# Kernel optimization log

Measured on AMD Instinct MI355X. Metric: run time of the kernel, lower is better.

The kernel has to match this reference:

```python
import jax, jax.numpy as jnp
import numpy as np

N_ATOMS = 50000
N_RES = 6250
C_IN = 30
E_DIM = 12
E_BOND = 150000
E_RAD = 800000
E_RES_RAD = 400000
E_CORR = 20000


def _layer_norm(h, g, b, eps=1e-5):
    mu = h.mean(-1, keepdims=True)
    var = ((h - mu) ** 2).mean(-1, keepdims=True)
    return (h - mu) / jnp.sqrt(var + eps) * g + b


def _mlp(h, W, b, g, beta):
    # Seq(Linear, ReLU, LayerNorm, Dropout) in eval mode (dropout = identity)
    return _layer_norm(jax.nn.relu(h @ W + b), g, beta)


def _point_conv(x, pos, src, dst, W, b, g, beta, num_nodes):
    # PyG PointNetConv with add_self_loops=True, aggr='add'
    loops = jnp.arange(num_nodes)
    s = jnp.concatenate([src, loops])
    d = jnp.concatenate([dst, loops])
    msg = jnp.concatenate([x[s], pos[s] - pos[d]], axis=-1)  # [E+N, F+3]
    h = _mlp(msg, W, b, g, beta)
    return jax.ops.segment_sum(h, d, num_segments=num_nodes)


def _gcne_conv(x, edge_index, edge_attr, W, bias):
    # GCNEConv: gcn_norm with self loops, message = cat(x_j, e) @ W * norm + bias, scatter-add
    n = x.shape[0]
    loops = jnp.arange(n)
    s = jnp.concatenate([edge_index[0], loops])
    d = jnp.concatenate([edge_index[1], loops])
    w_full = jnp.ones(s.shape[0], x.dtype)
    deg = jax.ops.segment_sum(w_full, d, num_segments=n)
    dinv = jnp.where(deg > 0, deg ** -0.5, 0.0)
    norm = dinv[s] * dinv[d]
    ea = jnp.concatenate([edge_attr, jnp.zeros((n, edge_attr.shape[1]), edge_attr.dtype)], axis=0)
    msg = (jnp.concatenate([x[s], ea], axis=-1) @ W) * norm[:, None] + bias
    return jax.ops.segment_sum(msg, d, num_segments=n)


def setup_inputs():
    key = jax.random.key(0)
    ks = jax.random.split(key, 20)
    inp = {}
    inp['x'] = jax.random.normal(ks[0], (N_ATOMS, C_IN), jnp.float32)
    inp['pos'] = jax.random.uniform(ks[1], (N_ATOMS, 3), jnp.float32)
    inp['edge_attr'] = jax.random.normal(ks[2], (E_BOND, E_DIM), jnp.float32)
    inp['edge_index'] = jax.random.randint(ks[3], (2, E_BOND), 0, N_ATOMS)
    inp['rad_edge_index'] = jax.random.randint(ks[4], (2, E_RAD), 0, N_ATOMS)
    inp['res_rad_edge_index'] = jax.random.randint(ks[5], (2, E_RES_RAD), 0, N_RES)
    inp['residue_index'] = jnp.sort(jax.random.randint(ks[6], (N_ATOMS,), 0, N_RES))
    inp['src_idx'] = jax.random.randint(ks[7], (E_CORR,), 0, N_RES)
    inp['tgt_idx'] = jax.random.randint(ks[8], (E_CORR,), 0, N_RES)
    inp['y_lab'] = jax.random.randint(ks[9], (E_CORR,), 0, 2).astype(jnp.int32)
    def glorot(k, shape):
        s = (2.0 / (shape[0] + shape[1])) ** 0.5
        return jax.random.normal(k, shape, jnp.float32) * s
    # conv1 local MLP [3+C_IN -> 64]
    inp['w_pc1'] = glorot(ks[10], (C_IN + 3, 64)); inp['b_pc1'] = jnp.zeros(64)
    inp['g_pc1'] = jnp.ones(64); inp['be_pc1'] = jnp.zeros(64)
    # gcn1 weight [C_IN+E_DIM -> 64]
    inp['w_gcn'] = glorot(ks[11], (C_IN + E_DIM, 64)); inp['b_gcn'] = jnp.zeros(64)
    # atom_embed MLP [64 -> 64]
    inp['w_ae'] = glorot(ks[12], (64, 64)); inp['b_ae'] = jnp.zeros(64)
    inp['g_ae'] = jnp.ones(64); inp['be_ae'] = jnp.zeros(64)
    # res_embed MLP [64 -> 64]
    inp['w_re'] = glorot(ks[13], (64, 64)); inp['b_re'] = jnp.zeros(64)
    inp['g_re'] = jnp.ones(64); inp['be_re'] = jnp.zeros(64)
    # res_conv1 local MLP [3+64 -> 128]
    inp['w_rc'] = glorot(ks[14], (64 + 3, 128)); inp['b_rc'] = jnp.zeros(128)
    inp['g_rc'] = jnp.ones(128); inp['be_rc'] = jnp.zeros(128)
    # res_conv1 global MLP [128 -> 128]
    inp['w_rg'] = glorot(ks[15], (128, 128)); inp['b_rg'] = jnp.zeros(128)
    inp['g_rg'] = jnp.ones(128); inp['be_rg'] = jnp.zeros(128)
    return inp


def reference(x, pos, edge_attr,
              w_pc1, b_pc1, g_pc1, be_pc1,
              w_gcn, b_gcn,
              w_ae, b_ae, g_ae, be_ae,
              w_re, b_re, g_re, be_re,
              w_rc, b_rc, g_rc, be_rc,
              w_rg, b_rg, g_rg, be_rg,
              edge_index, rad_edge_index, res_rad_edge_index,
              residue_index, src_idx, tgt_idx, y_lab):
    n = x.shape[0]
    # SAModule 1: PointConv over atom radius graph, aggr='add', no global_nn
    x1 = _point_conv(x, pos, rad_edge_index[0], rad_edge_index[1],
                     w_pc1, b_pc1, g_pc1, be_pc1, n)
    # GCNEConv over bond graph
    x2 = _gcne_conv(x, edge_index, edge_attr, w_gcn, b_gcn)
    atom_x = _mlp(x1 + x2, w_ae, b_ae, g_ae, be_ae)
    # atom -> residue pooling (global_add_pool / global_mean_pool)
    res_x = jax.ops.segment_sum(atom_x, residue_index, num_segments=N_RES)
    cnt = jax.ops.segment_sum(jnp.ones(n, x.dtype), residue_index, num_segments=N_RES)
    res_pos = jax.ops.segment_sum(pos, residue_index, num_segments=N_RES) / jnp.maximum(cnt, 1.0)[:, None]
    res_x = _mlp(res_x, w_re, b_re, g_re, be_re)
    # SAModule 2: PointConv over residue radius graph with global MLP
    x3 = _point_conv(res_x, res_pos, res_rad_edge_index[0], res_rad_edge_index[1],
                     w_rc, b_rc, g_rc, be_rc, N_RES)
    x3 = _mlp(x3, w_rg, b_rg, g_rg, be_rg)
    # correspondence pairs + CosineEmbeddingLoss(reduction='none')
    x_s = x3[src_idx]
    x_t = x3[tgt_idx]
    y = (2 * y_lab - 1).astype(x.dtype)  # {0,1} -> {-1,+1}
    eps = 1e-8
    cos = (x_s * x_t).sum(-1) / (jnp.maximum(jnp.linalg.norm(x_s, axis=-1), eps) *
                                 jnp.maximum(jnp.linalg.norm(x_t, axis=-1), eps))
    unweighted = jnp.where(y == 1, 1.0 - cos, jnp.maximum(cos, 0.0))
    pos_l = jnp.where(y != 1, 0.0, y)
    neg_l = 1.0 - pos_l
    pos_w = neg_l.sum() / pos_l.sum()
    loss = jnp.mean((pos_l * pos_w + neg_l) * unweighted)
    return loss
```

## Files before the change

### kernel.cpp

```cpp
#include <hip/hip_runtime.h>
#include <math.h>

#define N_ATOMS 50000
#define N_RES 6250
#define C_IN 30
#define E_DIM 12
#define E_BOND 150000
#define E_RAD 800000
#define E_RES_RAD 400000
#define E_CORR 20000

__device__ __forceinline__ int rfl(int v) { return __builtin_amdgcn_readfirstlane(v); }

template <int K>
__global__ void rowmat64(const float* __restrict__ X, const float* __restrict__ W,
                         float* __restrict__ out, int nrows) {
  const int lane = threadIdx.x & 63;
  const int wid = (blockIdx.x * blockDim.x + threadIdx.x) >> 6;
  const int nw = (gridDim.x * blockDim.x) >> 6;
  float wcol[K];
#pragma unroll
  for (int k = 0; k < K; k++) wcol[k] = W[k * 64 + lane];
  for (int r = wid; r < nrows; r += nw) {
    float acc = 0.0f;
#pragma unroll
    for (int k = 0; k < K; k++) acc += X[(size_t)r * K + k] * wcol[k];
    out[(size_t)r * 64 + lane] = acc;
  }
}

__global__ void hist_kernel(const int* __restrict__ dst, int* __restrict__ cnt, int n) {
  int i = blockIdx.x * blockDim.x + threadIdx.x;
  if (i < n) atomicAdd(&cnt[dst[i]], 1);
}

__global__ void ex_scan(const int* __restrict__ cnt, int* __restrict__ cur, int n) {
  __shared__ int wsums[16];
  __shared__ int carry_s;
  const int tid = threadIdx.x;
  const int lane = tid & 63;
  const int w = tid >> 6;
  if (tid == 0) carry_s = 0;
  __syncthreads();
  for (int base = 0; base < n; base += 1024) {
    int i = base + tid;
    int v = (i < n) ? cnt[i] : 0;
    int s = v;
#pragma unroll
    for (int m = 1; m < 64; m <<= 1) {
      int t = __shfl_up(s, m, 64);
      if (lane >= m) s += t;
    }
    if (lane == 63) wsums[w] = s;
    __syncthreads();
    if (w == 0) {
      int x = (lane < 16) ? wsums[lane] : 0;
#pragma unroll
      for (int m = 1; m < 16; m <<= 1) {
        int t = __shfl_up(x, m, 64);
        if (lane >= m) x += t;
      }
      if (lane < 16) wsums[lane] = x;
    }
    __syncthreads();
    const int woff = (w > 0) ? wsums[w - 1] : 0;
    const int carry = carry_s;
    if (i < n) cur[i] = carry + woff + (s - v);
    __syncthreads();
    if (tid == 1023) carry_s = carry + wsums[15];
    __syncthreads();
  }
}

__global__ void scat_kernel(const int* __restrict__ src, const int* __restrict__ dst,
                            int* __restrict__ cur, int* __restrict__ ss, int n) {
  int e = blockIdx.x * blockDim.x + threadIdx.x;
  if (e < n) {
    int p = atomicAdd(&cur[dst[e]], 1);
    ss[p] = src[e];
  }
}

__global__ void pc1_gather(const float* __restrict__ xw1, const float* __restrict__ pos,
                           const int* __restrict__ ss, const int* __restrict__ cur,
                           const float* __restrict__ W, const float* __restrict__ b,
                           const float* __restrict__ g, const float* __restrict__ be,
                           float* __restrict__ acc) {
  const int lane = threadIdx.x & 63;
  const int d = (blockIdx.x * blockDim.x + threadIdx.x) >> 6;
  if (d >= N_ATOMS) return;
  const float w0 = W[(C_IN + 0) * 64 + lane];
  const float w1 = W[(C_IN + 1) * 64 + lane];
  const float w2 = W[(C_IN + 2) * 64 + lane];
  const float bb = b[lane], gg = g[lane], eb = be[lane];
  const int beg = rfl(d ? cur[d - 1] : 0);
  const int end = rfl(cur[d]);
  const float pd0 = pos[d * 3 + 0], pd1 = pos[d * 3 + 1], pd2 = pos[d * 3 + 2];
  float h = fmaxf(xw1[(size_t)d * 64 + lane] + bb, 0.0f);
  float s1 = h, s2 = h * h;
#pragma unroll
  for (int m = 1; m < 64; m <<= 1) {
    s1 += __shfl_xor(s1, m, 64);
    s2 += __shfl_xor(s2, m, 64);
  }
  float mu = s1 * (1.0f / 64.0f);
  float var = s2 * (1.0f / 64.0f) - mu * mu;
  float accv = (h - mu) * rsqrtf(var + 1e-5f) * gg + eb;
  int j = beg;
  for (; j + 1 < end; j += 2) {
    const int sA = rfl(ss[j]);
    const int sB = rfl(ss[j + 1]);
    const float dA0 = pos[sA * 3 + 0] - pd0, dA1 = pos[sA * 3 + 1] - pd1,
                dA2 = pos[sA * 3 + 2] - pd2;
    const float dB0 = pos[sB * 3 + 0] - pd0, dB1 = pos[sB * 3 + 1] - pd1,
                dB2 = pos[sB * 3 + 2] - pd2;
    float hA = fmaxf(xw1[(size_t)sA * 64 + lane] + bb + dA0 * w0 + dA1 * w1 + dA2 * w2, 0.0f);
    float hB = fmaxf(xw1[(size_t)sB * 64 + lane] + bb + dB0 * w0 + dB1 * w1 + dB2 * w2, 0.0f);
    float s1A = hA, s2A = hA * hA, s1B = hB, s2B = hB * hB;
#pragma unroll
    for (int m = 1; m < 64; m <<= 1) {
      s1A += __shfl_xor(s1A, m, 64);
      s2A += __shfl_xor(s2A, m, 64);
      s1B += __shfl_xor(s1B, m, 64);
      s2B += __shfl_xor(s2B, m, 64);
    }
    const float muA = s1A * (1.0f / 64.0f), muB = s1B * (1.0f / 64.0f);
    const float vaA = s2A * (1.0f / 64.0f) - muA * muA;
    const float vaB = s2B * (1.0f / 64.0f) - muB * muB;
    accv += (hA - muA) * rsqrtf(vaA + 1e-5f) * gg + eb;
    accv += (hB - muB) * rsqrtf(vaB + 1e-5f) * gg + eb;
  }
  if (j < end) {
    const int sA = rfl(ss[j]);
    const float dA0 = pos[sA * 3 + 0] - pd0, dA1 = pos[sA * 3 + 1] - pd1,
                dA2 = pos[sA * 3 + 2] - pd2;
    float hA = fmaxf(xw1[(size_t)sA * 64 + lane] + bb + dA0 * w0 + dA1 * w1 + dA2 * w2, 0.0f);
    float s1A = hA, s2A = hA * hA;
#pragma unroll
    for (int m = 1; m < 64; m <<= 1) {
      s1A += __shfl_xor(s1A, m, 64);
      s2A += __shfl_xor(s2A, m, 64);
    }
    const float muA = s1A * (1.0f / 64.0f);
    const float vaA = s2A * (1.0f / 64.0f) - muA * muA;
    accv += (hA - muA) * rsqrtf(vaA + 1e-5f) * gg + eb;
  }
  acc[(size_t)d * 64 + lane] = accv;
}

__global__ void deg_init(float* __restrict__ deg) {
  int i = blockIdx.x * blockDim.x + threadIdx.x;
  if (i < N_ATOMS) deg[i] = 1.0f;
}
__global__ void deg_count(const int* __restrict__ dst, float* __restrict__ deg) {
  int i = blockIdx.x * blockDim.x + threadIdx.x;
  if (i < E_BOND) atomicAdd(&deg[dst[i]], 1.0f);
}
__global__ void deg_inv(float* __restrict__ deg) {
  int i = blockIdx.x * blockDim.x + threadIdx.x;
  if (i < N_ATOMS) deg[i] = rsqrtf(deg[i]);
}

__global__ void gcn_edge(const float* __restrict__ xw2, const float* __restrict__ ea,
                         const int* __restrict__ src, const int* __restrict__ dst,
                         const float* __restrict__ W, const float* __restrict__ b,
                         const float* __restrict__ dinv, float* __restrict__ acc) {
  const int lane = threadIdx.x & 63;
  const int wid = (blockIdx.x * blockDim.x + threadIdx.x) >> 6;
  const int nw = (gridDim.x * blockDim.x) >> 6;
  float we[E_DIM];
#pragma unroll
  for (int k = 0; k < E_DIM; k++) we[k] = W[(C_IN + k) * 64 + lane];
  const float bb = b[lane];
  for (int e = wid; e < E_BOND; e += nw) {
    int s = rfl(src[e]);
    int d = rfl(dst[e]);
    float t = xw2[(size_t)s * 64 + lane];
#pragma unroll
    for (int k = 0; k < E_DIM; k++) t += ea[(size_t)e * E_DIM + k] * we[k];
    t = t * (dinv[s] * dinv[d]) + bb;
    atomicAdd(&acc[(size_t)d * 64 + lane], t);
  }
}

__global__ void atom_embed(const float* __restrict__ acc12, const float* __restrict__ xw2,
                           const float* __restrict__ dinv, const float* __restrict__ bgcn,
                           const float* __restrict__ pos, const int* __restrict__ resid,
                           const float* __restrict__ W, const float* __restrict__ b,
                           const float* __restrict__ g, const float* __restrict__ be,
                           float* __restrict__ res_acc, float* __restrict__ res_pacc,
                           float* __restrict__ res_cnt) {
  const int lane = threadIdx.x & 63;
  const int wid = (blockIdx.x * blockDim.x + threadIdx.x) >> 6;
  const int nw = (gridDim.x * blockDim.x) >> 6;
  const float bb = b[lane], gg = g[lane], eb = be[lane], bg = bgcn[lane];
  for (int r = wid; r < N_ATOMS; r += nw) {
    const float di = dinv[r];
    float vin = acc12[(size_t)r * 64 + lane] + xw2[(size_t)r * 64 + lane] * di * di + bg;
    float acc = bb;
#pragma unroll 8
    for (int k = 0; k < 64; k++) {
      float xv = __shfl(vin, k, 64);
      acc += xv * W[k * 64 + lane];
    }
    float h = fmaxf(acc, 0.0f);
    float s1 = h, s2 = h * h;
#pragma unroll
    for (int m = 1; m < 64; m <<= 1) {
      s1 += __shfl_xor(s1, m, 64);
      s2 += __shfl_xor(s2, m, 64);
    }
    float mu = s1 * (1.0f / 64.0f);
    float var = s2 * (1.0f / 64.0f) - mu * mu;
    float v = (h - mu) * rsqrtf(var + 1e-5f) * gg + eb;
    int rr = resid[r];
    atomicAdd(&res_acc[(size_t)rr * 64 + lane], v);
    if (lane < 3) atomicAdd(&res_pacc[rr * 3 + lane], pos[r * 3 + lane]);
    if (lane == 3) atomicAdd(&res_cnt[rr], 1.0f);
  }
}

__global__ void res_embed(const float* __restrict__ racc, const float* __restrict__ pacc,
                          const float* __restrict__ cnt, const float* __restrict__ W,
                          const float* __restrict__ b, const float* __restrict__ g,
                          const float* __restrict__ be, float* __restrict__ res_x,
                          float* __restrict__ res_pos) {
  const int lane = threadIdx.x & 63;
  const int wid = (blockIdx.x * blockDim.x + threadIdx.x) >> 6;
  const int nw = (gridDim.x * blockDim.x) >> 6;
  const float bb = b[lane], gg = g[lane], eb = be[lane];
  for (int r = wid; r < N_RES; r += nw) {
    float vin = racc[(size_t)r * 64 + lane];
    float acc = bb;
#pragma unroll 8
    for (int k = 0; k < 64; k++) {
      float xv = __shfl(vin, k, 64);
      acc += xv * W[k * 64 + lane];
    }
    float h = fmaxf(acc, 0.0f);
    float s1 = h, s2 = h * h;
#pragma unroll
    for (int m = 1; m < 64; m <<= 1) {
      s1 += __shfl_xor(s1, m, 64);
      s2 += __shfl_xor(s2, m, 64);
    }
    float mu = s1 * (1.0f / 64.0f);
    float var = s2 * (1.0f / 64.0f) - mu * mu;
    res_x[(size_t)r * 64 + lane] = (h - mu) * rsqrtf(var + 1e-5f) * gg + eb;
    if (lane < 3) res_pos[r * 3 + lane] = pacc[r * 3 + lane] / fmaxf(cnt[r], 1.0f);
  }
}

__global__ void rc_pre(const float* __restrict__ rx, const float* __restrict__ W,
                       const float* __restrict__ b, float* __restrict__ rw) {
  const int lane = threadIdx.x & 63;
  const int wid = (blockIdx.x * blockDim.x + threadIdx.x) >> 6;
  const int nw = (gridDim.x * blockDim.x) >> 6;
  for (int r = wid; r < N_RES; r += nw) {
    float vin = rx[(size_t)r * 64 + lane];
    float a0 = b[lane], a1 = b[64 + lane];
#pragma unroll 8
    for (int k = 0; k < 64; k++) {
      float xv = __shfl(vin, k, 64);
      a0 += xv * W[k * 128 + lane];
      a1 += xv * W[k * 128 + 64 + lane];
    }
    rw[(size_t)r * 128 + lane] = a0;
    rw[(size_t)r * 128 + 64 + lane] = a1;
  }
}

__global__ void rc_gather(const float* __restrict__ rw, const float* __restrict__ rpos,
                          const int* __restrict__ ss, const int* __restrict__ cur,
                          const float* __restrict__ W, const float* __restrict__ g,
                          const float* __restrict__ be, float* __restrict__ out) {
  const int lane = threadIdx.x & 63;
  const int d = (blockIdx.x * blockDim.x + threadIdx.x) >> 6;
  if (d >= N_RES) return;
  float wa[3], wb[3];
#pragma unroll
  for (int i = 0; i < 3; i++) {
    wa[i] = W[(64 + i) * 128 + lane];
    wb[i] = W[(64 + i) * 128 + 64 + lane];
  }
  const float g0 = g[lane], g1 = g[64 + lane], e0c = be[lane], e1c = be[64 + lane];
  const int beg = rfl(d ? cur[d - 1] : 0);
  const int end = rfl(cur[d]);
  const float pd0 = rpos[d * 3 + 0], pd1 = rpos[d * 3 + 1], pd2 = rpos[d * 3 + 2];
  float h0 = fmaxf(rw[(size_t)d * 128 + lane], 0.0f);
  float h1 = fmaxf(rw[(size_t)d * 128 + 64 + lane], 0.0f);
  float s1 = h0 + h1, s2 = h0 * h0 + h1 * h1;
#pragma unroll
  for (int m = 1; m < 64; m <<= 1) {
    s1 += __shfl_xor(s1, m, 64);
    s2 += __shfl_xor(s2, m, 64);
  }
  float mu = s1 * (1.0f / 128.0f);
  float var = s2 * (1.0f / 128.0f) - mu * mu;
  float rs = rsqrtf(var + 1e-5f);
  float a0 = (h0 - mu) * rs * g0 + e0c;
  float a1 = (h1 - mu) * rs * g1 + e1c;
  int j = beg;
  for (; j + 1 < end; j += 2) {
    const int sA = rfl(ss[j]);
    const int sB = rfl(ss[j + 1]);
    const float dA0 = rpos[sA * 3 + 0] - pd0, dA1 = rpos[sA * 3 + 1] - pd1,
                dA2 = rpos[sA * 3 + 2] - pd2;
    const float dB0 = rpos[sB * 3 + 0] - pd0, dB1 = rpos[sB * 3 + 1] - pd1,
                dB2 = rpos[sB * 3 + 2] - pd2;
    float hA0 = fmaxf(rw[(size_t)sA * 128 + lane]      + dA0 * wa[0] + dA1 * wa[1] + dA2 * wa[2], 0.0f);
    float hA1 = fmaxf(rw[(size_t)sA * 128 + 64 + lane] + dA0 * wb[0] + dA1 * wb[1] + dA2 * wb[2], 0.0f);
    float hB0 = fmaxf(rw[(size_t)sB * 128 + lane]      + dB0 * wa[0] + dB1 * wa[1] + dB2 * wa[2], 0.0f);
    float hB1 = fmaxf(rw[(size_t)sB * 128 + 64 + lane] + dB0 * wb[0] + dB1 * wb[1] + dB2 * wb[2], 0.0f);
    float s1A = hA0 + hA1, s2A = hA0 * hA0 + hA1 * hA1;
    float s1B = hB0 + hB1, s2B = hB0 * hB0 + hB1 * hB1;
#pragma unroll
    for (int m = 1; m < 64; m <<= 1) {
      s1A += __shfl_xor(s1A, m, 64);
      s2A += __shfl_xor(s2A, m, 64);
      s1B += __shfl_xor(s1B, m, 64);
      s2B += __shfl_xor(s2B, m, 64);
    }
    const float muA = s1A * (1.0f / 128.0f), muB = s1B * (1.0f / 128.0f);
    const float vaA = s2A * (1.0f / 128.0f) - muA * muA;
    const float vaB = s2B * (1.0f / 128.0f) - muB * muB;
    const float rsA = rsqrtf(vaA + 1e-5f), rsB = rsqrtf(vaB + 1e-5f);
    a0 += (hA0 - muA) * rsA * g0 + e0c + (hB0 - muB) * rsB * g0 + e0c;
    a1 += (hA1 - muA) * rsA * g1 + e1c + (hB1 - muB) * rsB * g1 + e1c;
  }
  if (j < end) {
    const int sA = rfl(ss[j]);
    const float dA0 = rpos[sA * 3 + 0] - pd0, dA1 = rpos[sA * 3 + 1] - pd1,
                dA2 = rpos[sA * 3 + 2] - pd2;
    float hA0 = fmaxf(rw[(size_t)sA * 128 + lane]      + dA0 * wa[0] + dA1 * wa[1] + dA2 * wa[2], 0.0f);
    float hA1 = fmaxf(rw[(size_t)sA * 128 + 64 + lane] + dA0 * wb[0] + dA1 * wb[1] + dA2 * wb[2], 0.0f);
    float s1A = hA0 + hA1, s2A = hA0 * hA0 + hA1 * hA1;
#pragma unroll
    for (int m = 1; m < 64; m <<= 1) {
      s1A += __shfl_xor(s1A, m, 64);
      s2A += __shfl_xor(s2A, m, 64);
    }
    const float muA = s1A * (1.0f / 128.0f);
    const float vaA = s2A * (1.0f / 128.0f) - muA * muA;
    const float rsA = rsqrtf(vaA + 1e-5f);
    a0 += (hA0 - muA) * rsA * g0 + e0c;
    a1 += (hA1 - muA) * rsA * g1 + e1c;
  }
  out[(size_t)d * 128 + lane] = a0;
  out[(size_t)d * 128 + 64 + lane] = a1;
}

__global__ void rg_embed(const float* __restrict__ acc, const float* __restrict__ W,
                         const float* __restrict__ b, const float* __restrict__ g,
                         const float* __restrict__ be, float* __restrict__ x3) {
  const int lane = threadIdx.x & 63;
  const int wid = (blockIdx.x * blockDim.x + threadIdx.x) >> 6;
  const int nw = (gridDim.x * blockDim.x) >> 6;
  for (int r = wid; r < N_RES; r += nw) {
    float i0 = acc[(size_t)r * 128 + lane];
    float i1 = acc[(size_t)r * 128 + 64 + lane];
    float a0 = b[lane], a1 = b[64 + lane];
#pragma unroll 8
    for (int k = 0; k < 64; k++) {
      float x0 = __shfl(i0, k, 64);
      float x1 = __shfl(i1, k, 64);
      a0 += x0 * W[k * 128 + lane] + x1 * W[(k + 64) * 128 + lane];
      a1 += x0 * W[k * 128 + 64 + lane] + x1 * W[(k + 64) * 128 + 64 + lane];
    }
    float h0 = fmaxf(a0, 0.0f), h1 = fmaxf(a1, 0.0f);
    float s1 = h0 + h1, s2 = h0 * h0 + h1 * h1;
#pragma unroll
    for (int m = 1; m < 64; m <<= 1) {
      s1 += __shfl_xor(s1, m, 64);
      s2 += __shfl_xor(s2, m, 64);
    }
    float mu = s1 * (1.0f / 128.0f);
    float var = s2 * (1.0f / 128.0f) - mu * mu;
    float rs = rsqrtf(var + 1e-5f);
    x3[(size_t)r * 128 + lane] = (h0 - mu) * rs * g[lane] + be[lane];
    x3[(size_t)r * 128 + 64 + lane] = (h1 - mu) * rs * g[64 + lane] + be[64 + lane];
  }
}

__global__ void loss_pairs(const float* __restrict__ x3, const int* __restrict__ si,
                           const int* __restrict__ ti, const int* __restrict__ y,
                           float* __restrict__ lacc) {
  const int lane = threadIdx.x & 63;
  const int wid = (blockIdx.x * blockDim.x + threadIdx.x) >> 6;
  const int nw = (gridDim.x * blockDim.x) >> 6;
  float sp = 0.0f, sn = 0.0f, cp = 0.0f, cn = 0.0f;
  for (int p = wid; p < E_CORR; p += nw) {
    int a = rfl(si[p]), bI = rfl(ti[p]), yy = rfl(y[p]);
    float a0 = x3[(size_t)a * 128 + lane], a1 = x3[(size_t)a * 128 + 64 + lane];
    float b0 = x3[(size_t)bI * 128 + lane], b1 = x3[(size_t)bI * 128 + 64 + lane];
    float dot = a0 * b0 + a1 * b1;
    float na = a0 * a0 + a1 * a1;
    float nb = b0 * b0 + b1 * b1;
#pragma unroll
    for (int m = 1; m < 64; m <<= 1) {
      dot += __shfl_xor(dot, m, 64);
      na += __shfl_xor(na, m, 64);
      nb += __shfl_xor(nb, m, 64);
    }
    float cosv = dot / (fmaxf(sqrtf(na), 1e-8f) * fmaxf(sqrtf(nb), 1e-8f));
    if (yy == 1) {
      sp += 1.0f - cosv;
      cp += 1.0f;
    } else {
      sn += fmaxf(cosv, 0.0f);
      cn += 1.0f;
    }
  }
  if (lane == 0) {
    atomicAdd(&lacc[0], sp);
    atomicAdd(&lacc[1], sn);
    atomicAdd(&lacc[2], cp);
    atomicAdd(&lacc[3], cn);
  }
}

__global__ void finalize(const float* __restrict__ lacc, float* __restrict__ out) {
  if (blockIdx.x == 0 && threadIdx.x == 0) {
    float pw = lacc[3] / lacc[2];
    out[0] = (lacc[0] * pw + lacc[1]) / (float)E_CORR;
  }
}

extern "C" void kernel_launch(void* const* d_in, const int* in_sizes, int n_in,
                              void* d_out, int out_size, void* d_ws, size_t ws_size,
                              hipStream_t stream) {
  const float* x = (const float*)d_in[0];
  const float* pos = (const float*)d_in[1];
  const float* edge_attr = (const float*)d_in[2];
  const int* edge_index = (const int*)d_in[3];
  const int* rad_ei = (const int*)d_in[4];
  const int* res_rad_ei = (const int*)d_in[5];
  const int* resid = (const int*)d_in[6];
  const int* src_idx = (const int*)d_in[7];
  const int* tgt_idx = (const int*)d_in[8];
  const int* y_lab = (const int*)d_in[9];
  const float* w_pc1 = (const float*)d_in[10];
  const float* b_pc1 = (const float*)d_in[11];
  const float* g_pc1 = (const float*)d_in[12];
  const float* be_pc1 = (const float*)d_in[13];
  const float* w_gcn = (const float*)d_in[14];
  const float* b_gcn = (const float*)d_in[15];
  const float* w_ae = (const float*)d_in[16];
  const float* b_ae = (const float*)d_in[17];
  const float* g_ae = (const float*)d_in[18];
  const float* be_ae = (const float*)d_in[19];
  const float* w_re = (const float*)d_in[20];
  const float* b_re = (const float*)d_in[21];
  const float* g_re = (const float*)d_in[22];
  const float* be_re = (const float*)d_in[23];
  const float* w_rc = (const float*)d_in[24];
  const float* b_rc = (const float*)d_in[25];
  const float* g_rc = (const float*)d_in[26];
  const float* be_rc = (const float*)d_in[27];
  const float* w_rg = (const float*)d_in[28];
  const float* b_rg = (const float*)d_in[29];
  const float* g_rg = (const float*)d_in[30];
  const float* be_rg = (const float*)d_in[31];

  float* ws = (float*)d_ws;
  float* res_acc = ws;
  float* res_pacc = res_acc + 400000;
  float* res_cnt = res_pacc + 18752;
  float* lacc = res_cnt + 6272;
  int* cnt_pc1 = (int*)(lacc + 8);
  int* cnt_rc = cnt_pc1 + 50048;
  size_t zero_elems = 400000 + 18752 + 6272 + 8 + 50048 + 6272;
  int* cur_pc1 = cnt_rc + 6272;
  int* cur_rc = cur_pc1 + 50048;
  int* ss_pc1 = cur_rc + 6272;
  int* ss_rc = ss_pc1 + 800000;
  float* xw1 = (float*)(ss_rc + 400000);
  float* xw2 = xw1 + 3200000;
  float* deg = xw2 + 3200000;
  float* acc12 = deg + 50000;
  float* res_x = acc12 + 3200000;
  float* res_pos = res_x + 400000;
  float* rw = res_pos + 18752;
  float* x3m = acc12;
  float* x3 = rw;

  hipMemsetAsync(d_ws, 0, zero_elems * sizeof(float), stream);

  const int B = 256;
  const int GB = 2048;
  const int GS = 512;

  rowmat64<C_IN><<<GB, B, 0, stream>>>(x, w_pc1, xw1, N_ATOMS);
  rowmat64<C_IN><<<GB, B, 0, stream>>>(x, w_gcn, xw2, N_ATOMS);

  hist_kernel<<<(E_RAD + B - 1) / B, B, 0, stream>>>(rad_ei + E_RAD, cnt_pc1, E_RAD);
  ex_scan<<<1, 1024, 0, stream>>>(cnt_pc1, cur_pc1, N_ATOMS);
  scat_kernel<<<(E_RAD + B - 1) / B, B, 0, stream>>>(rad_ei, rad_ei + E_RAD, cur_pc1,
                                                     ss_pc1, E_RAD);
  pc1_gather<<<(N_ATOMS * 64 + B - 1) / B, B, 0, stream>>>(xw1, pos, ss_pc1, cur_pc1,
                                                           w_pc1, b_pc1, g_pc1, be_pc1,
                                                           acc12);

  deg_init<<<(N_ATOMS + B - 1) / B, B, 0, stream>>>(deg);
  deg_count<<<(E_BOND + B - 1) / B, B, 0, stream>>>(edge_index + E_BOND, deg);
  deg_inv<<<(N_ATOMS + B - 1) / B, B, 0, stream>>>(deg);

  gcn_edge<<<GB, B, 0, stream>>>(xw2, edge_attr, edge_index, edge_index + E_BOND, w_gcn,
                                 b_gcn, deg, acc12);

  atom_embed<<<GB, B, 0, stream>>>(acc12, xw2, deg, b_gcn, pos, resid, w_ae, b_ae, g_ae,
                                   be_ae, res_acc, res_pacc, res_cnt);

  res_embed<<<GS, B, 0, stream>>>(res_acc, res_pacc, res_cnt, w_re, b_re, g_re, be_re,
                                  res_x, res_pos);

  hist_kernel<<<(E_RES_RAD + B - 1) / B, B, 0, stream>>>(res_rad_ei + E_RES_RAD, cnt_rc,
                                                         E_RES_RAD);
  ex_scan<<<1, 1024, 0, stream>>>(cnt_rc, cur_rc, N_RES);
  scat_kernel<<<(E_RES_RAD + B - 1) / B, B, 0, stream>>>(res_rad_ei,
                                                         res_rad_ei + E_RES_RAD, cur_rc,
                                                         ss_rc, E_RES_RAD);

  rc_pre<<<GS, B, 0, stream>>>(res_x, w_rc, b_rc, rw);
  rc_gather<<<(N_RES * 64 + B - 1) / B, B, 0, stream>>>(rw, res_pos, ss_rc, cur_rc, w_rc,
                                                        g_rc, be_rc, x3m);
  rg_embed<<<GS, B, 0, stream>>>(x3m, w_rg, b_rg, g_rg, be_rg, x3);

  loss_pairs<<<GS, B, 0, stream>>>(x3, src_idx, tgt_idx, y_lab, lacc);
  finalize<<<1, 64, 0, stream>>>(lacc, (float*)d_out);
}
```

Measured before the change: 790.7 us.

## Merge CSR builds for both graphs and split residue gather across four waves

The histogram, scan and scatter kernels for the atom and residue radius graphs are merged into single launches, and the scan processes four elements per thread. The pc1 gather loop is unrolled to four edges per iteration for more memory-level parallelism. rc_gather now assigns four waves per residue, each handling a chunk of the edge list and atomically adding into a zeroed accumulator. This trades extra float atomics, a larger memset and nondeterministic summation order for more parallelism on the heavy residue graph (about 64 edges per node).

```diff
diff --git a/kernel.cpp b/kernel.cpp
--- a/kernel.cpp
+++ b/kernel.cpp
@@ -29,12 +29,22 @@
   }
 }
 
-__global__ void hist_kernel(const int* __restrict__ dst, int* __restrict__ cnt, int n) {
+__global__ void hist2(const int* __restrict__ d0, int* __restrict__ c0, int n0,
+                      const int* __restrict__ d1, int* __restrict__ c1, int n1) {
   int i = blockIdx.x * blockDim.x + threadIdx.x;
-  if (i < n) atomicAdd(&cnt[dst[i]], 1);
-}
-
-__global__ void ex_scan(const int* __restrict__ cnt, int* __restrict__ cur, int n) {
+  if (i < n0) {
+    atomicAdd(&c0[d0[i]], 1);
+  } else {
+    int k = i - n0;
+    if (k < n1) atomicAdd(&c1[d1[k]], 1);
+  }
+}
+
+__global__ void dual_scan(const int* __restrict__ c0, int* __restrict__ u0, int n0,
+                          const int* __restrict__ c1, int* __restrict__ u1, int n1) {
+  const int* cnt = blockIdx.x ? c1 : c0;
+  int* cur = blockIdx.x ? u1 : u0;
+  const int n = blockIdx.x ? n1 : n0;
   __shared__ int wsums[16];
   __shared__ int carry_s;
   const int tid = threadIdx.x;
@@ -42,10 +52,14 @@
   const int w = tid >> 6;
   if (tid == 0) carry_s = 0;
   __syncthreads();
-  for (int base = 0; base < n; base += 1024) {
-    int i = base + tid;
-    int v = (i < n) ? cnt[i] : 0;
-    int s = v;
+  for (int base = 0; base < n; base += 4096) {
+    const int i0 = base + tid * 4;
+    int v0 = (i0 + 0 < n) ? cnt[i0 + 0] : 0;
+    int v1 = (i0 + 1 < n) ? cnt[i0 + 1] : 0;
+    int v2 = (i0 + 2 < n) ? cnt[i0 + 2] : 0;
+    int v3 = (i0 + 3 < n) ? cnt[i0 + 3] : 0;
+    const int t0 = v0, t1 = t0 + v1, t2 = t1 + v2, t3 = t2 + v3;
+    int s = t3;
 #pragma unroll
     for (int m = 1; m < 64; m <<= 1) {
       int t = __shfl_up(s, m, 64);
@@ -64,20 +78,31 @@
     }
     __syncthreads();
     const int woff = (w > 0) ? wsums[w - 1] : 0;
-    const int carry = carry_s;
-    if (i < n) cur[i] = carry + woff + (s - v);
+    const int off = carry_s + woff + (s - t3);
+    if (i0 + 0 < n) cur[i0 + 0] = off;
+    if (i0 + 1 < n) cur[i0 + 1] = off + t0;
+    if (i0 + 2 < n) cur[i0 + 2] = off + t1;
+    if (i0 + 3 < n) cur[i0 + 3] = off + t2;
     __syncthreads();
-    if (tid == 1023) carry_s = carry + wsums[15];
+    if (tid == 1023) carry_s += wsums[15];
     __syncthreads();
   }
 }
 
-__global__ void scat_kernel(const int* __restrict__ src, const int* __restrict__ dst,
-                            int* __restrict__ cur, int* __restrict__ ss, int n) {
-  int e = blockIdx.x * blockDim.x + threadIdx.x;
-  if (e < n) {
-    int p = atomicAdd(&cur[dst[e]], 1);
-    ss[p] = src[e];
+__global__ void scat2(const int* __restrict__ s0, const int* __restrict__ d0,
+                      int* __restrict__ u0, int* __restrict__ o0, int n0,
+                      const int* __restrict__ s1, const int* __restrict__ d1,
+                      int* __restrict__ u1, int* __restrict__ o1, int n1) {
+  int i = blockIdx.x * blockDim.x + threadIdx.x;
+  if (i < n0) {
+    int p = atomicAdd(&u0[d0[i]], 1);
+    o0[p] = s0[i];
+  } else {
+    int k = i - n0;
+    if (k < n1) {
+      int p = atomicAdd(&u1[d1[k]], 1);
+      o1[p] = s1[k];
+    }
   }
 }
 
@@ -97,52 +122,86 @@
   const int end = rfl(cur[d]);
   const float pd0 = pos[d * 3 + 0], pd1 = pos[d * 3 + 1], pd2 = pos[d * 3 + 2];
   float h = fmaxf(xw1[(size_t)d * 64 + lane] + bb, 0.0f);
-  float s1 = h, s2 = h * h;
+  float p1 = h, p2 = h * h;
 #pragma unroll
   for (int m = 1; m < 64; m <<= 1) {
-    s1 += __shfl_xor(s1, m, 64);
-    s2 += __shfl_xor(s2, m, 64);
-  }
-  float mu = s1 * (1.0f / 64.0f);
-  float var = s2 * (1.0f / 64.0f) - mu * mu;
+    p1 += __shfl_xor(p1, m, 64);
+    p2 += __shfl_xor(p2, m, 64);
+  }
+  float mu = p1 * (1.0f / 64.0f);
+  float var = p2 * (1.0f / 64.0f) - mu * mu;
   float accv = (h - mu) * rsqrtf(var + 1e-5f) * gg + eb;
   int j = beg;
+  for (; j + 3 < end; j += 4) {
+    const int sA = rfl(ss[j]);
+    const int sB = rfl(ss[j + 1]);
+    const int sC = rfl(ss[j + 2]);
+    const int sD = rfl(ss[j + 3]);
+    const float dA0 = pos[sA * 3 + 0] - pd0, dA1 = pos[sA * 3 + 1] - pd1, dA2 = pos[sA * 3 + 2] - pd2;
+    const float dB0 = pos[sB * 3 + 0] - pd0, dB1 = pos[sB * 3 + 1] - pd1, dB2 = pos[sB * 3 + 2] - pd2;
+    const float dC0 = pos[sC * 3 + 0] - pd0, dC1 = pos[sC * 3 + 1] - pd1, dC2 = pos[sC * 3 + 2] - pd2;
+    const float dD0 = pos[sD * 3 + 0] - pd0, dD1 = pos[sD * 3 + 1] - pd1, dD2 = pos[sD * 3 + 2] - pd2;
+    float hA = fmaxf(xw1[(size_t)sA * 64 + lane] + bb + dA0 * w0 + dA1 * w1 + dA2 * w2, 0.0f);
+    float hB = fmaxf(xw1[(size_t)sB * 64 + lane] + bb + dB0 * w0 + dB1 * w1 + dB2 * w2, 0.0f);
+    float hC = fmaxf(xw1[(size_t)sC * 64 + lane] + bb + dC0 * w0 + dC1 * w1 + dC2 * w2, 0.0f);
+    float hD = fmaxf(xw1[(size_t)sD * 64 + lane] + bb + dD0 * w0 + dD1 * w1 + dD2 * w2, 0.0f);
+    float p1A = hA, p2A = hA * hA, p1B = hB, p2B = hB * hB;
+    float p1C = hC, p2C = hC * hC, p1D = hD, p2D = hD * hD;
+#pragma unroll
+    for (int m = 1; m < 64; m <<= 1) {
+      p1A += __shfl_xor(p1A, m, 64);
+      p2A += __shfl_xor(p2A, m, 64);
+      p1B += __shfl_xor(p1B, m, 64);
+      p2B += __shfl_xor(p2B, m, 64);
+      p1C += __shfl_xor(p1C, m, 64);
+      p2C += __shfl_xor(p2C, m, 64);
+      p1D += __shfl_xor(p1D, m, 64);
+      p2D += __shfl_xor(p2D, m, 64);
+    }
+    const float muA = p1A * (1.0f / 64.0f), muB = p1B * (1.0f / 64.0f);
+    const float muC = p1C * (1.0f / 64.0f), muD = p1D * (1.0f / 64.0f);
+    const float vaA = p2A * (1.0f / 64.0f) - muA * muA;
+    const float vaB = p2B * (1.0f / 64.0f) - muB * muB;
+    const float vaC = p2C * (1.0f / 64.0f) - muC * muC;
+    const float vaD = p2D * (1.0f / 64.0f) - muD * muD;
+    accv += (hA - muA) * rsqrtf(vaA + 1e-5f) * gg + eb;
+    accv += (hB - muB) * rsqrtf(vaB + 1e-5f) * gg + eb;
+    accv += (hC - muC) * rsqrtf(vaC + 1e-5f) * gg + eb;
+    accv += (hD - muD) * rsqrtf(vaD + 1e-5f) * gg + eb;
+  }
   for (; j + 1 < end; j += 2) {
     const int sA = rfl(ss[j]);
     const int sB = rfl(ss[j + 1]);
-    const float dA0 = pos[sA * 3 + 0] - pd0, dA1 = pos[sA * 3 + 1] - pd1,
-                dA2 = pos[sA * 3 + 2] - pd2;
-    const float dB0 = pos[sB * 3 + 0] - pd0, dB1 = pos[sB * 3 + 1] - pd1,
-                dB2 = pos[sB * 3 + 2] - pd2;
+    const float dA0 = pos[sA * 3 + 0] - pd0, dA1 = pos[sA * 3 + 1] - pd1, dA2 = pos[sA * 3 + 2] - pd2;
+    const float dB0 = pos[sB * 3 + 0] - pd0, dB1 = pos[sB * 3 + 1] - pd1, dB2 = pos[sB * 3 + 2] - pd2;
     float hA = fmaxf(xw1[(size_t)sA * 64 + lane] + bb + dA0 * w0 + dA1 * w1 + dA2 * w2, 0.0f);
     float hB = fmaxf(xw1[(size_t)sB * 64 + lane] + bb + dB0 * w0 + dB1 * w1 + dB2 * w2, 0.0f);
-    float s1A = hA, s2A = hA * hA, s1B = hB, s2B = hB * hB;
-#pragma unroll
-    for (int m = 1; m < 64; m <<= 1) {
-      s1A += __shfl_xor(s1A, m, 64);
-      s2A += __shfl_xor(s2A, m, 64);
-      s1B += __shfl_xor(s1B, m, 64);
-      s2B += __shfl_xor(s2B, m, 64);
-    }
-    const float muA = s1A * (1.0f / 64.0f), muB = s1B * (1.0f / 64.0f);
-    const float vaA = s2A * (1.0f / 64.0f) - muA * muA;
-    const float vaB = s2B * (1.0f / 64.0f) - muB * muB;
+    float p1A = hA, p2A = hA * hA, p1B = hB, p2B = hB * hB;
+#pragma unroll
+    for (int m = 1; m < 64; m <<= 1) {
+      p1A += __shfl_xor(p1A, m, 64);
+      p2A += __shfl_xor(p2A, m, 64);
+      p1B += __shfl_xor(p1B, m, 64);
+      p2B += __shfl_xor(p2B, m, 64);
+    }
+    const float muA = p1A * (1.0f / 64.0f), muB = p1B * (1.0f / 64.0f);
+    const float vaA = p2A * (1.0f / 64.0f) - muA * muA;
+    const float vaB = p2B * (1.0f / 64.0f) - muB * muB;
     accv += (hA - muA) * rsqrtf(vaA + 1e-5f) * gg + eb;
     accv += (hB - muB) * rsqrtf(vaB + 1e-5f) * gg + eb;
   }
   if (j < end) {
     const int sA = rfl(ss[j]);
-    const float dA0 = pos[sA * 3 + 0] - pd0, dA1 = pos[sA * 3 + 1] - pd1,
-                dA2 = pos[sA * 3 + 2] - pd2;
+    const float dA0 = pos[sA * 3 + 0] - pd0, dA1 = pos[sA * 3 + 1] - pd1, dA2 = pos[sA * 3 + 2] - pd2;
     float hA = fmaxf(xw1[(size_t)sA * 64 + lane] + bb + dA0 * w0 + dA1 * w1 + dA2 * w2, 0.0f);
-    float s1A = hA, s2A = hA * hA;
-#pragma unroll
-    for (int m = 1; m < 64; m <<= 1) {
-      s1A += __shfl_xor(s1A, m, 64);
-      s2A += __shfl_xor(s2A, m, 64);
-    }
-    const float muA = s1A * (1.0f / 64.0f);
-    const float vaA = s2A * (1.0f / 64.0f) - muA * muA;
+    float p1A = hA, p2A = hA * hA;
+#pragma unroll
+    for (int m = 1; m < 64; m <<= 1) {
+      p1A += __shfl_xor(p1A, m, 64);
+      p2A += __shfl_xor(p2A, m, 64);
+    }
+    const float muA = p1A * (1.0f / 64.0f);
+    const float vaA = p2A * (1.0f / 64.0f) - muA * muA;
     accv += (hA - muA) * rsqrtf(vaA + 1e-5f) * gg + eb;
   }
   acc[(size_t)d * 64 + lane] = accv;
@@ -270,12 +329,15 @@
   }
 }
 
+#define RPW 4
 __global__ void rc_gather(const float* __restrict__ rw, const float* __restrict__ rpos,
                           const int* __restrict__ ss, const int* __restrict__ cur,
                           const float* __restrict__ W, const float* __restrict__ g,
                           const float* __restrict__ be, float* __restrict__ out) {
   const int lane = threadIdx.x & 63;
-  const int d = (blockIdx.x * blockDim.x + threadIdx.x) >> 6;
+  const int gw = (blockIdx.x * blockDim.x + threadIdx.x) >> 6;
+  const int d = gw >> 2;
+  const int q = gw & 3;
   if (d >= N_RES) return;
   float wa[3], wb[3];
 #pragma unroll
@@ -286,68 +348,71 @@
   const float g0 = g[lane], g1 = g[64 + lane], e0c = be[lane], e1c = be[64 + lane];
   const int beg = rfl(d ? cur[d - 1] : 0);
   const int end = rfl(cur[d]);
+  const int len = end - beg;
+  const int chunk = (len + RPW - 1) >> 2;
+  int j = beg + q * chunk;
+  const int je = min(j + chunk, end);
   const float pd0 = rpos[d * 3 + 0], pd1 = rpos[d * 3 + 1], pd2 = rpos[d * 3 + 2];
-  float h0 = fmaxf(rw[(size_t)d * 128 + lane], 0.0f);
-  float h1 = fmaxf(rw[(size_t)d * 128 + 64 + lane], 0.0f);
-  float s1 = h0 + h1, s2 = h0 * h0 + h1 * h1;
-#pragma unroll
-  for (int m = 1; m < 64; m <<= 1) {
-    s1 += __shfl_xor(s1, m, 64);
-    s2 += __shfl_xor(s2, m, 64);
-  }
-  float mu = s1 * (1.0f / 128.0f);
-  float var = s2 * (1.0f / 128.0f) - mu * mu;
-  float rs = rsqrtf(var + 1e-5f);
-  float a0 = (h0 - mu) * rs * g0 + e0c;
-  float a1 = (h1 - mu) * rs * g1 + e1c;
-  int j = beg;
-  for (; j + 1 < end; j += 2) {
+  float a0 = 0.0f, a1 = 0.0f;
+  if (q == 0) {
+    float h0 = fmaxf(rw[(size_t)d * 128 + lane], 0.0f);
+    float h1 = fmaxf(rw[(size_t)d * 128 + 64 + lane], 0.0f);
+    float p1 = h0 + h1, p2 = h0 * h0 + h1 * h1;
+#pragma unroll
+    for (int m = 1; m < 64; m <<= 1) {
+      p1 += __shfl_xor(p1, m, 64);
+      p2 += __shfl_xor(p2, m, 64);
+    }
+    float mu = p1 * (1.0f / 128.0f);
+    float var = p2 * (1.0f / 128.0f) - mu * mu;
+    float rs = rsqrtf(var + 1e-5f);
+    a0 = (h0 - mu) * rs * g0 + e0c;
+    a1 = (h1 - mu) * rs * g1 + e1c;
+  }
+  for (; j + 1 < je; j += 2) {
     const int sA = rfl(ss[j]);
     const int sB = rfl(ss[j + 1]);
-    const float dA0 = rpos[sA * 3 + 0] - pd0, dA1 = rpos[sA * 3 + 1] - pd1,
-                dA2 = rpos[sA * 3 + 2] - pd2;
-    const float dB0 = rpos[sB * 3 + 0] - pd0, dB1 = rpos[sB * 3 + 1] - pd1,
-                dB2 = rpos[sB * 3 + 2] - pd2;
+    const float dA0 = rpos[sA * 3 + 0] - pd0, dA1 = rpos[sA * 3 + 1] - pd1, dA2 = rpos[sA * 3 + 2] - pd2;
+    const float dB0 = rpos[sB * 3 + 0] - pd0, dB1 = rpos[sB * 3 + 1] - pd1, dB2 = rpos[sB * 3 + 2] - pd2;
     float hA0 = fmaxf(rw[(size_t)sA * 128 + lane]      + dA0 * wa[0] + dA1 * wa[1] + dA2 * wa[2], 0.0f);
     float hA1 = fmaxf(rw[(size_t)sA * 128 + 64 + lane] + dA0 * wb[0] + dA1 * wb[1] + dA2 * wb[2], 0.0f);
     float hB0 = fmaxf(rw[(size_t)sB * 128 + lane]      + dB0 * wa[0] + dB1 * wa[1] + dB2 * wa[2], 0.0f);
     float hB1 = fmaxf(rw[(size_t)sB * 128 + 64 + lane] + dB0 * wb[0] + dB1 * wb[1] + dB2 * wb[2], 0.0f);
-    float s1A = hA0 + hA1, s2A = hA0 * hA0 + hA1 * hA1;
-    float s1B = hB0 + hB1, s2B = hB0 * hB0 + hB1 * hB1;
-#pragma unroll
-    for (int m = 1; m < 64; m <<= 1) {
-      s1A += __shfl_xor(s1A, m, 64);
-      s2A += __shfl_xor(s2A, m, 64);
-      s1B += __shfl_xor(s1B, m, 64);
-      s2B += __shfl_xor(s2B, m, 64);
-    }
-    const float muA = s1A * (1.0f / 128.0f), muB = s1B * (1.0f / 128.0f);
-    const float vaA = s2A * (1.0f / 128.0f) - muA * muA;
-    const float vaB = s2B * (1.0f / 128.0f) - muB * muB;
+    float p1A = hA0 + hA1, p2A = hA0 * hA0 + hA1 * hA1;
+    float p1B = hB0 + hB1, p2B = hB0 * hB0 + hB1 * hB1;
+#pragma unroll
+    for (int m = 1; m < 64; m <<= 1) {
+      p1A += __shfl_xor(p1A, m, 64);
+      p2A += __shfl_xor(p2A, m, 64);
+      p1B += __shfl_xor(p1B, m, 64);
+      p2B += __shfl_xor(p2B, m, 64);
+    }
+    const float muA = p1A * (1.0f / 128.0f), muB = p1B * (1.0f / 128.0f);
+    const float vaA = p2A * (1.0f / 128.0f) - muA * muA;
+    const float vaB = p2B * (1.0f / 128.0f) - muB * muB;
     const float rsA = rsqrtf(vaA + 1e-5f), rsB = rsqrtf(vaB + 1e-5f);
     a0 += (hA0 - muA) * rsA * g0 + e0c + (hB0 - muB) * rsB * g0 + e0c;
     a1 += (hA1 - muA) * rsA * g1 + e1c + (hB1 - muB) * rsB * g1 + e1c;
   }
-  if (j < end) {
+  if (j < je) {
     const int sA = rfl(ss[j]);
-    const float dA0 = rpos[sA * 3 + 0] - pd0, dA1 = rpos[sA * 3 + 1] - pd1,
-                dA2 = rpos[sA * 3 + 2] - pd2;
+    const float dA0 = rpos[sA * 3 + 0] - pd0, dA1 = rpos[sA * 3 + 1] - pd1, dA2 = rpos[sA * 3 + 2] - pd2;
     float hA0 = fmaxf(rw[(size_t)sA * 128 + lane]      + dA0 * wa[0] + dA1 * wa[1] + dA2 * wa[2], 0.0f);
     float hA1 = fmaxf(rw[(size_t)sA * 128 + 64 + lane] + dA0 * wb[0] + dA1 * wb[1] + dA2 * wb[2], 0.0f);
-    float s1A = hA0 + hA1, s2A = hA0 * hA0 + hA1 * hA1;
-#pragma unroll
-    for (int m = 1; m < 64; m <<= 1) {
-      s1A += __shfl_xor(s1A, m, 64);
-      s2A += __shfl_xor(s2A, m, 64);
-    }
-    const float muA = s1A * (1.0f / 128.0f);
-    const float vaA = s2A * (1.0f / 128.0f) - muA * muA;
+    float p1A = hA0 + hA1, p2A = hA0 * hA0 + hA1 * hA1;
+#pragma unroll
+    for (int m = 1; m < 64; m <<= 1) {
+      p1A += __shfl_xor(p1A, m, 64);
+      p2A += __shfl_xor(p2A, m, 64);
+    }
+    const float muA = p1A * (1.0f / 128.0f);
+    const float vaA = p2A * (1.0f / 128.0f) - muA * muA;
     const float rsA = rsqrtf(vaA + 1e-5f);
     a0 += (hA0 - muA) * rsA * g0 + e0c;
     a1 += (hA1 - muA) * rsA * g1 + e1c;
   }
-  out[(size_t)d * 128 + lane] = a0;
-  out[(size_t)d * 128 + 64 + lane] = a1;
+  atomicAdd(&out[(size_t)d * 128 + lane], a0);
+  atomicAdd(&out[(size_t)d * 128 + 64 + lane], a1);
 }
 
 __global__ void rg_embed(const float* __restrict__ acc, const float* __restrict__ W,
@@ -469,8 +534,9 @@
   float* lacc = res_cnt + 6272;
   int* cnt_pc1 = (int*)(lacc + 8);
   int* cnt_rc = cnt_pc1 + 50048;
-  size_t zero_elems = 400000 + 18752 + 6272 + 8 + 50048 + 6272;
-  int* cur_pc1 = cnt_rc + 6272;
+  float* x3acc = (float*)(cnt_rc + 6272);
+  size_t zero_elems = 400000 + 18752 + 6272 + 8 + 50048 + 6272 + 800000;
+  int* cur_pc1 = (int*)(x3acc + 800000);
   int* cur_rc = cur_pc1 + 50048;
   int* ss_pc1 = cur_rc + 6272;
   int* ss_rc = ss_pc1 + 800000;
@@ -481,7 +547,6 @@
   float* res_x = acc12 + 3200000;
   float* res_pos = res_x + 400000;
   float* rw = res_pos + 18752;
-  float* x3m = acc12;
   float* x3 = rw;
 
   hipMemsetAsync(d_ws, 0, zero_elems * sizeof(float), stream);
@@ -493,10 +558,13 @@
   rowmat64<C_IN><<<GB, B, 0, stream>>>(x, w_pc1, xw1, N_ATOMS);
   rowmat64<C_IN><<<GB, B, 0, stream>>>(x, w_gcn, xw2, N_ATOMS);
 
-  hist_kernel<<<(E_RAD + B - 1) / B, B, 0, stream>>>(rad_ei + E_RAD, cnt_pc1, E_RAD);
-  ex_scan<<<1, 1024, 0, stream>>>(cnt_pc1, cur_pc1, N_ATOMS);
-  scat_kernel<<<(E_RAD + B - 1) / B, B, 0, stream>>>(rad_ei, rad_ei + E_RAD, cur_pc1,
-                                                     ss_pc1, E_RAD);
+  hist2<<<(E_RAD + E_RES_RAD + B - 1) / B, B, 0, stream>>>(
+      rad_ei + E_RAD, cnt_pc1, E_RAD, res_rad_ei + E_RES_RAD, cnt_rc, E_RES_RAD);
+  dual_scan<<<2, 1024, 0, stream>>>(cnt_pc1, cur_pc1, N_ATOMS, cnt_rc, cur_rc, N_RES);
+  scat2<<<(E_RAD + E_RES_RAD + B - 1) / B, B, 0, stream>>>(
+      rad_ei, rad_ei + E_RAD, cur_pc1, ss_pc1, E_RAD,
+      res_rad_ei, res_rad_ei + E_RES_RAD, cur_rc, ss_rc, E_RES_RAD);
+
   pc1_gather<<<(N_ATOMS * 64 + B - 1) / B, B, 0, stream>>>(xw1, pos, ss_pc1, cur_pc1,
                                                            w_pc1, b_pc1, g_pc1, be_pc1,
                                                            acc12);
@@ -514,17 +582,10 @@
   res_embed<<<GS, B, 0, stream>>>(res_acc, res_pacc, res_cnt, w_re, b_re, g_re, be_re,
                                   res_x, res_pos);
 
-  hist_kernel<<<(E_RES_RAD + B - 1) / B, B, 0, stream>>>(res_rad_ei + E_RES_RAD, cnt_rc,
-                                                         E_RES_RAD);
-  ex_scan<<<1, 1024, 0, stream>>>(cnt_rc, cur_rc, N_RES);
-  scat_kernel<<<(E_RES_RAD + B - 1) / B, B, 0, stream>>>(res_rad_ei,
-                                                         res_rad_ei + E_RES_RAD, cur_rc,
-                                                         ss_rc, E_RES_RAD);
-
   rc_pre<<<GS, B, 0, stream>>>(res_x, w_rc, b_rc, rw);
-  rc_gather<<<(N_RES * 64 + B - 1) / B, B, 0, stream>>>(rw, res_pos, ss_rc, cur_rc, w_rc,
-                                                        g_rc, be_rc, x3m);
-  rg_embed<<<GS, B, 0, stream>>>(x3m, w_rg, b_rg, g_rg, be_rg, x3);
+  rc_gather<<<(N_RES * RPW * 64 + B - 1) / B, B, 0, stream>>>(rw, res_pos, ss_rc, cur_rc,
+                                                              w_rc, g_rc, be_rc, x3acc);
+  rg_embed<<<GS, B, 0, stream>>>(x3acc, w_rg, b_rg, g_rg, be_rg, x3);
 
   loss_pairs<<<GS, B, 0, stream>>>(x3, src_idx, tgt_idx, y_lab, lacc);
   finalize<<<1, 64, 0, stream>>>(lacc, (float*)d_out);
```

Measured after the change: 747.4 us. 1.06x faster.
